# Kernel tuning notes

Measured on AMD Instinct MI355X. Metric: run time of the kernel, lower is better.

Reference implementation:

```python
import jax, jax.numpy as jnp
import numpy as np

N_HEAD = 16
N_EMBD = 1024

def setup_inputs() -> dict:
    key = jax.random.key(0)
    ks = jax.random.split(key, 7)
    B, S, D = 2, 2048, N_EMBD
    scale = 1.0 / np.sqrt(D)
    return {
        "x": jax.random.normal(ks[0], (B, S, D), dtype=jnp.float32),
        "Wq": jax.random.normal(ks[1], (D, D), dtype=jnp.float32) * scale,
        "bq": jnp.zeros((D,), dtype=jnp.float32),
        "Wk": jax.random.normal(ks[2], (D, D), dtype=jnp.float32) * scale,
        "bk": jnp.zeros((D,), dtype=jnp.float32),
        "Wv": jax.random.normal(ks[3], (D, D), dtype=jnp.float32) * scale,
        "bv": jnp.zeros((D,), dtype=jnp.float32),
    }

def reference(x, Wq, bq, Wk, bk, Wv, bv):
    B, S, D = x.shape
    H = N_HEAD
    hd = D // H
    # QKV projections
    q = (x @ Wq + bq).reshape(B, S, H, hd).transpose(0, 2, 1, 3)  # [B,H,S,hd]
    k = (x @ Wk + bk).reshape(B, S, H, hd).transpose(0, 2, 1, 3)
    v = (x @ Wv + bv).reshape(B, S, H, hd).transpose(0, 2, 1, 3)
    # Note: original module defines a causal mask but never applies it.
    att = jnp.einsum("bhqd,bhkd->bhqk", q, k) * (1.0 / jnp.sqrt(hd).astype(x.dtype))
    att = jax.nn.softmax(att, axis=-1)
    y = jnp.einsum("bhqk,bhkd->bhqd", att, v)  # [B,H,S,hd]
    return y.transpose(0, 2, 1, 3).reshape(B, S, D)
```

## Files before the change

### kernel.cpp

```cpp
#include <hip/hip_runtime.h>


#define D_MODEL 1024
#define NHEAD   16
#define HDIM    64
#define SEQ     2048
#define MROWS   4096
#define CSC     0.18033688011112042f

typedef __attribute__((ext_vector_type(8))) short short8;
typedef __attribute__((ext_vector_type(4))) float f32x4;

__device__ __forceinline__ float bf2f(unsigned short u) {
  return __uint_as_float(((unsigned int)u) << 16);
}
__device__ __forceinline__ unsigned short f2bf(float f) {
  unsigned int u = __float_as_uint(f);
  u += 0x7fff + ((u >> 16) & 1);
  return (unsigned short)(u >> 16);
}
__device__ __forceinline__ unsigned int cvtpk_bf16(float lo, float hi) {
  unsigned int r;
  asm("v_cvt_pk_bf16_f32 %0, %1, %2" : "=v"(r) : "v"(lo), "v"(hi));
  return r;
}

__device__ __forceinline__ int sniff_bf16(const unsigned short* x) {
  int cnt = 0;
#pragma unroll
  for (int i = 0; i < 64; ++i) {
    const unsigned e = (x[2 * i] >> 7) & 0xFF;
    cnt += (e >= 105 && e <= 140) ? 1 : 0;
  }
  return cnt >= 48;
}

__device__ __forceinline__ void gl_lds16(const unsigned short* g, unsigned short* l) {
  __builtin_amdgcn_global_load_lds(
      (const __attribute__((address_space(1))) unsigned int*)g,
      (__attribute__((address_space(3))) unsigned int*)l, 16, 0, 0);
}

__global__ __launch_bounds__(256) void cvt_x(const unsigned short* __restrict__ X,
                                             unsigned short* __restrict__ Xbf) {
  const int isbf = sniff_bf16(X);
  const size_t i0 = ((size_t)blockIdx.x * 256 + threadIdx.x) * 8;
  if (isbf) {
    *(uint4*)(Xbf + i0) = *(const uint4*)(X + i0);
  } else {
    const float* Xf = (const float*)X;
    const float4 f0 = *(const float4*)(Xf + i0);
    const float4 f1 = *(const float4*)(Xf + i0 + 4);
    unsigned int t[4] = {cvtpk_bf16(f0.x, f0.y), cvtpk_bf16(f0.z, f0.w),
                         cvtpk_bf16(f1.x, f1.y), cvtpk_bf16(f1.z, f1.w)};
    *(uint4*)(Xbf + i0) = *(const uint4*)t;
  }
}

__global__ __launch_bounds__(256) void cvt_w(
    const unsigned short* __restrict__ w0, const unsigned short* __restrict__ w1,
    const unsigned short* __restrict__ w2,
    const unsigned short* __restrict__ b0, const unsigned short* __restrict__ b1,
    const unsigned short* __restrict__ b2,
    unsigned short* __restrict__ Wt, unsigned short* __restrict__ bb) {
  __shared__ unsigned short tile[32][33];
  const int z = blockIdx.z;
  const unsigned short* W    = (z == 0) ? w0 : ((z == 1) ? w1 : w2);
  const unsigned short* bias = (z == 0) ? b0 : ((z == 1) ? b1 : b2);
  unsigned short* Wtz = Wt + ((size_t)z << 20);
  const int isbf = sniff_bf16(W);
  const int bx = blockIdx.x * 32;
  const int by = blockIdx.y * 32;
  const int tx = threadIdx.x & 31;
  const int ty = threadIdx.x >> 5;
#pragma unroll
  for (int r = ty; r < 32; r += 8) {
    unsigned short v;
    if (isbf) v = W[(size_t)(by + r) * D_MODEL + bx + tx];
    else      v = f2bf(((const float*)W)[(size_t)(by + r) * D_MODEL + bx + tx]);
    tile[r][tx] = v;
  }
  __syncthreads();
#pragma unroll
  for (int r = ty; r < 32; r += 8)
    Wtz[(size_t)(bx + r) * D_MODEL + by + tx] = tile[tx][r];
  if (blockIdx.x == 0 && blockIdx.y == 0) {
    const int i0 = threadIdx.x * 4;
#pragma unroll
    for (int j = 0; j < 4; ++j)
      bb[z * D_MODEL + i0 + j] =
          isbf ? bias[i0 + j] : f2bf(((const float*)bias)[i0 + j]);
  }
}

__device__ __forceinline__ void store_cd(int z, unsigned short* Out, int row0,
                                         int col, const f32x4 acc, float bb,
                                         float sc) {
  if (z == 2) {
    const int b = row0 >> 11, s = row0 & 2047;
    const int bh = b * NHEAD + (col >> 6);
    uint2 pk;
    pk.x = cvtpk_bf16(acc[0] + bb, acc[1] + bb);
    pk.y = cvtpk_bf16(acc[2] + bb, acc[3] + bb);
    *(uint2*)(Out + ((size_t)bh * HDIM + (col & 63)) * SEQ + s) = pk;
  } else {
#pragma unroll
    for (int r = 0; r < 4; ++r)
      Out[(size_t)(row0 + r) * D_MODEL + col] = f2bf((acc[r] + bb) * sc);
  }
}

__global__ __launch_bounds__(256) void qkv_gemm_fast(
    const unsigned short* __restrict__ Xbf, const unsigned short* __restrict__ Wt,
    const unsigned short* __restrict__ bb,
    unsigned short* __restrict__ Oq, unsigned short* __restrict__ Ok,
    unsigned short* __restrict__ Ov) {
  const int z = blockIdx.z;
  const unsigned short* Wz = Wt + ((size_t)z << 20);
  unsigned short* Out = (z == 0) ? Oq : ((z == 1) ? Ok : Ov);
  const float sc = (z == 0) ? CSC : 1.0f;

  __shared__ unsigned short As[128 * 32];
  __shared__ unsigned short Bs[128 * 32];

  const int tid  = threadIdx.x;
  const int wave = tid >> 6, lane = tid & 63;
  const int wm = wave >> 1, wn = wave & 1;
  const int lrow = lane & 15, lk = lane >> 4;
  const int m0 = blockIdx.y * 128;
  const int n0 = blockIdx.x * 128;

  f32x4 acc[4][4] = {};

  for (int kk = 0; kk < D_MODEL; kk += 32) {
#pragma unroll
    for (int i = 0; i < 2; ++i) {
      const int c = i * 256 + tid;
      const int row = c >> 2, off = (c & 3) * 8;
      gl_lds16(Xbf + (size_t)(m0 + row) * D_MODEL + kk + off, &As[c * 8]);
      gl_lds16(Wz  + (size_t)(n0 + row) * D_MODEL + kk + off, &Bs[c * 8]);
    }
    __syncthreads();
    short8 a[4], b[4];
#pragma unroll
    for (int t = 0; t < 4; ++t) {
      a[t] = *(const short8*)(&As[(wm * 64 + t * 16 + lrow) * 32 + lk * 8]);
      b[t] = *(const short8*)(&Bs[(wn * 64 + t * 16 + lrow) * 32 + lk * 8]);
    }
#pragma unroll
    for (int mt = 0; mt < 4; ++mt)
#pragma unroll
      for (int nt = 0; nt < 4; ++nt)
        acc[mt][nt] = __builtin_amdgcn_mfma_f32_16x16x32_bf16(a[mt], b[nt], acc[mt][nt], 0, 0, 0);
    __syncthreads();
  }
#pragma unroll
  for (int nt = 0; nt < 4; ++nt) {
    const int col = n0 + wn * 64 + nt * 16 + lrow;
    const float bv = bf2f(bb[z * D_MODEL + col]);
#pragma unroll
    for (int mt = 0; mt < 4; ++mt)
      store_cd(z, Out, m0 + wm * 64 + mt * 16 + lk * 4, col, acc[mt][nt], bv, sc);
  }
}

#define LDA 40
__global__ __launch_bounds__(256) void qkv_gemm_med(
    const unsigned short* __restrict__ X, const unsigned short* __restrict__ Wt,
    const unsigned short* __restrict__ bb,
    unsigned short* __restrict__ Oq, unsigned short* __restrict__ Ok,
    unsigned short* __restrict__ Ov) {
  const int z = blockIdx.z;
  const unsigned short* Wz = Wt + ((size_t)z << 20);
  unsigned short* Out = (z == 0) ? Oq : ((z == 1) ? Ok : Ov);
  const float sc = (z == 0) ? CSC : 1.0f;

  __shared__ alignas(16) unsigned short As[128 * LDA];
  __shared__ alignas(16) unsigned short Bs[128 * LDA];

  const int isbf = sniff_bf16(X);
  const int tid  = threadIdx.x;
  const int wave = tid >> 6, lane = tid & 63;
  const int wm = wave >> 1, wn = wave & 1;
  const int lrow = lane & 15, lk = lane >> 4;
  const int m0 = blockIdx.y * 128;
  const int n0 = blockIdx.x * 128;

  f32x4 acc[4][4] = {};

  for (int kk = 0; kk < D_MODEL; kk += 32) {
#pragma unroll
    for (int i = 0; i < 2; ++i) {
      const int c = tid + i * 256;
      const int row = c >> 2, off = (c & 3) * 8;
      if (isbf) {
        *(uint4*)(&As[row * LDA + off]) =
            *(const uint4*)(X + (size_t)(m0 + row) * D_MODEL + kk + off);
      } else {
        const float* Xf = (const float*)X;
        const float4 f0 = *(const float4*)(Xf + (size_t)(m0 + row) * D_MODEL + kk + off);
        const float4 f1 = *(const float4*)(Xf + (size_t)(m0 + row) * D_MODEL + kk + off + 4);
        unsigned int t[4] = {cvtpk_bf16(f0.x, f0.y), cvtpk_bf16(f0.z, f0.w),
                             cvtpk_bf16(f1.x, f1.y), cvtpk_bf16(f1.z, f1.w)};
        *(uint4*)(&As[row * LDA + off]) = *(const uint4*)t;
      }
      *(uint4*)(&Bs[row * LDA + off]) =
          *(const uint4*)(Wz + (size_t)(n0 + row) * D_MODEL + kk + off);
    }
    __syncthreads();
    short8 a[4], b[4];
#pragma unroll
    for (int t = 0; t < 4; ++t) {
      a[t] = *(const short8*)(&As[(wm * 64 + t * 16 + lrow) * LDA + lk * 8]);
      b[t] = *(const short8*)(&Bs[(wn * 64 + t * 16 + lrow) * LDA + lk * 8]);
    }
#pragma unroll
    for (int mt = 0; mt < 4; ++mt)
#pragma unroll
      for (int nt = 0; nt < 4; ++nt)
        acc[mt][nt] = __builtin_amdgcn_mfma_f32_16x16x32_bf16(a[mt], b[nt], acc[mt][nt], 0, 0, 0);
    __syncthreads();
  }
#pragma unroll
  for (int nt = 0; nt < 4; ++nt) {
    const int col = n0 + wn * 64 + nt * 16 + lrow;
    const float bv = bf2f(bb[z * D_MODEL + col]);
#pragma unroll
    for (int mt = 0; mt < 4; ++mt)
      store_cd(z, Out, m0 + wm * 64 + mt * 16 + lk * 4, col, acc[mt][nt], bv, sc);
  }
}

__global__ __launch_bounds__(256) void qkv_gemm(
    const unsigned short* __restrict__ X,
    const unsigned short* __restrict__ Wq, const unsigned short* __restrict__ Wk,
    const unsigned short* __restrict__ Wv,
    const unsigned short* __restrict__ bq, const unsigned short* __restrict__ bk,
    const unsigned short* __restrict__ bv,
    unsigned short* __restrict__ Oq, unsigned short* __restrict__ Ok,
    unsigned short* __restrict__ Ov) {
  const int z = blockIdx.z;
  const unsigned short* W    = (z == 0) ? Wq : ((z == 1) ? Wk : Wv);
  const unsigned short* bias = (z == 0) ? bq : ((z == 1) ? bk : bv);
  unsigned short*       Out  = (z == 0) ? Oq : ((z == 1) ? Ok : Ov);
  const float sc = (z == 0) ? CSC : 1.0f;

  __shared__ alignas(16) unsigned short As[128 * LDA];
  __shared__ alignas(16) unsigned short Bs[128 * LDA];

  const int isbf = sniff_bf16(X);
  const int tid  = threadIdx.x;
  const int wave = tid >> 6, lane = tid & 63;
  const int wm = wave >> 1, wn = wave & 1;
  const int lrow = lane & 15, lk = lane >> 4;
  const int m0 = blockIdx.y * 128;
  const int n0 = blockIdx.x * 128;

  f32x4 acc[4][4] = {};

  for (int kk = 0; kk < D_MODEL; kk += 32) {
#pragma unroll
    for (int i = 0; i < 2; ++i) {
      const int c = tid + i * 256;
      const int row = c >> 2, off = (c & 3) * 8;
      if (isbf) {
        *(uint4*)(&As[row * LDA + off]) =
            *(const uint4*)(X + (size_t)(m0 + row) * D_MODEL + kk + off);
      } else {
        const float* Xf = (const float*)X;
        const float4 f0 = *(const float4*)(Xf + (size_t)(m0 + row) * D_MODEL + kk + off);
        const float4 f1 = *(const float4*)(Xf + (size_t)(m0 + row) * D_MODEL + kk + off + 4);
        unsigned int t[4] = {cvtpk_bf16(f0.x, f0.y), cvtpk_bf16(f0.z, f0.w),
                             cvtpk_bf16(f1.x, f1.y), cvtpk_bf16(f1.z, f1.w)};
        *(uint4*)(&As[row * LDA + off]) = *(const uint4*)t;
      }
    }
#pragma unroll
    for (int i = 0; i < 2; ++i) {
      const int c = tid + i * 256;
      const int krow = c & 31;
      const int nc0 = (c >> 5) * 8;
      if (isbf) {
        uint4 v = *(const uint4*)(W + (size_t)(kk + krow) * D_MODEL + n0 + nc0);
        const unsigned short* e = (const unsigned short*)&v;
#pragma unroll
        for (int j = 0; j < 8; ++j) Bs[(nc0 + j) * LDA + krow] = e[j];
      } else {
        const float* Wf = (const float*)W;
        const float4 f0 = *(const float4*)(Wf + (size_t)(kk + krow) * D_MODEL + n0 + nc0);
        const float4 f1 = *(const float4*)(Wf + (size_t)(kk + krow) * D_MODEL + n0 + nc0 + 4);
        const float vals[8] = {f0.x, f0.y, f0.z, f0.w, f1.x, f1.y, f1.z, f1.w};
#pragma unroll
        for (int j = 0; j < 8; ++j) Bs[(nc0 + j) * LDA + krow] = f2bf(vals[j]);
      }
    }
    __syncthreads();
    short8 a[4], b[4];
#pragma unroll
    for (int t = 0; t < 4; ++t) {
      a[t] = *(const short8*)(&As[(wm * 64 + t * 16 + lrow) * LDA + lk * 8]);
      b[t] = *(const short8*)(&Bs[(wn * 64 + t * 16 + lrow) * LDA + lk * 8]);
    }
#pragma unroll
    for (int mt = 0; mt < 4; ++mt)
#pragma unroll
      for (int nt = 0; nt < 4; ++nt)
        acc[mt][nt] = __builtin_amdgcn_mfma_f32_16x16x32_bf16(a[mt], b[nt], acc[mt][nt], 0, 0, 0);
    __syncthreads();
  }
#pragma unroll
  for (int nt = 0; nt < 4; ++nt) {
    const int col = n0 + wn * 64 + nt * 16 + lrow;
    const float bv2 = isbf ? bf2f(bias[col]) : ((const float*)bias)[col];
#pragma unroll
    for (int mt = 0; mt < 4; ++mt)
      store_cd(z, Out, m0 + wm * 64 + mt * 16 + lk * 4, col, acc[mt][nt], bv2, sc);
  }
}

#define LDK 72
__global__ __launch_bounds__(256) void attn(
    const unsigned short* __restrict__ Qg, const unsigned short* __restrict__ Kg,
    const unsigned short* __restrict__ Vtg, unsigned short* __restrict__ Outg,
    const unsigned short* __restrict__ Xs) {
  const int qt = blockIdx.x;
  const int bh = blockIdx.y;
  const int b = bh >> 4, h = bh & 15;
  const size_t baseR = (size_t)b * SEQ * D_MODEL + h * HDIM;
  const size_t baseV = (size_t)bh * HDIM * SEQ;

  __shared__ alignas(16) unsigned short Ks[64 * LDK];
  __shared__ alignas(16) unsigned short Vs[64 * LDK];
  __shared__ alignas(16) unsigned short Ps[128 * LDK];

  const int isbf = sniff_bf16(Xs);
  const int tid  = threadIdx.x;
  const int wave = tid >> 6, lane = tid & 63;
  const int lrow = lane & 15, lk = lane >> 4;
  const int q0 = qt * 128;
  const int wq = wave * 32;

  short8 qf[2][2];
#pragma unroll
  for (int nq = 0; nq < 2; ++nq)
#pragma unroll
    for (int ks = 0; ks < 2; ++ks)
      qf[nq][ks] = *(const short8*)(Qg + baseR +
          (size_t)(q0 + wq + nq * 16 + lrow) * D_MODEL + ks * 32 + lk * 8);

  f32x4 accO[2][4] = {};
  float lsum[2] = {0.f, 0.f};

  uint4 kreg[2], vreg[2];
  auto LOADT = [&](int kv) {
#pragma unroll
    for (int i = 0; i < 2; ++i) {
      const int c = tid + i * 256;
      const int row = c >> 3, off = (c & 7) * 8;
      kreg[i] = *(const uint4*)(Kg + baseR + (size_t)(kv + row) * D_MODEL + off);
      vreg[i] = *(const uint4*)(Vtg + baseV + (size_t)row * SEQ + kv + off);
    }
  };
  auto WRITET = [&]() {
#pragma unroll
    for (int i = 0; i < 2; ++i) {
      const int c = tid + i * 256;
      const int row = c >> 3, off = (c & 7) * 8;
      *(uint4*)(&Ks[row * LDK + off]) = kreg[i];
      *(uint4*)(&Vs[row * LDK + off]) = vreg[i];
    }
  };

  LOADT(0);
  WRITET();
  __syncthreads();

#pragma unroll 1
  for (int kv0 = 0; kv0 < SEQ; kv0 += 64) {
    const int nxt = kv0 + 64;
    if (nxt < SEQ) LOADT(nxt);

    f32x4 accST[4][2] = {};
#pragma unroll
    for (int ks = 0; ks < 2; ++ks) {
      short8 kf[4];
#pragma unroll
      for (int mt = 0; mt < 4; ++mt)
        kf[mt] = *(const short8*)(&Ks[(mt * 16 + lrow) * LDK + ks * 32 + lk * 8]);
#pragma unroll
      for (int mt = 0; mt < 4; ++mt)
#pragma unroll
        for (int nq = 0; nq < 2; ++nq)
          accST[mt][nq] = __builtin_amdgcn_mfma_f32_16x16x32_bf16(
              kf[mt], qf[nq][ks], accST[mt][nq], 0, 0, 0);
    }

#pragma unroll
    for (int mt = 0; mt < 4; ++mt)
#pragma unroll
      for (int nq = 0; nq < 2; ++nq) {
        const float p0 = exp2f(accST[mt][nq][0]), p1 = exp2f(accST[mt][nq][1]);
        const float p2 = exp2f(accST[mt][nq][2]), p3 = exp2f(accST[mt][nq][3]);
        lsum[nq] += (p0 + p1) + (p2 + p3);
        uint2 pk;
        pk.x = cvtpk_bf16(p0, p1);
        pk.y = cvtpk_bf16(p2, p3);
        *(uint2*)(&Ps[(wq + nq * 16 + lrow) * LDK + mt * 16 + lk * 4]) = pk;
      }

#pragma unroll
    for (int ks = 0; ks < 2; ++ks) {
      short8 pf[2], vf[4];
#pragma unroll
      for (int mq = 0; mq < 2; ++mq)
        pf[mq] = *(const short8*)(&Ps[(wq + mq * 16 + lrow) * LDK + ks * 32 + lk * 8]);
#pragma unroll
      for (int nd = 0; nd < 4; ++nd)
        vf[nd] = *(const short8*)(&Vs[(nd * 16 + lrow) * LDK + ks * 32 + lk * 8]);
#pragma unroll
      for (int mq = 0; mq < 2; ++mq)
#pragma unroll
        for (int nd = 0; nd < 4; ++nd)
          accO[mq][nd] = __builtin_amdgcn_mfma_f32_16x16x32_bf16(
              pf[mq], vf[nd], accO[mq][nd], 0, 0, 0);
    }

    __syncthreads();
    if (nxt < SEQ) WRITET();
    __syncthreads();
  }

#pragma unroll
  for (int nq = 0; nq < 2; ++nq) {
    lsum[nq] += __shfl_xor(lsum[nq], 16, 64);
    lsum[nq] += __shfl_xor(lsum[nq], 32, 64);
  }
  __syncthreads();
  float* Lf = (float*)Ps;
  if (lk == 0) {
    Lf[wq + lrow]      = lsum[0];
    Lf[wq + 16 + lrow] = lsum[1];
  }
#pragma unroll
  for (int mq = 0; mq < 2; ++mq) {
    const f32x4 l4 = *(const f32x4*)(&Lf[wq + mq * 16 + lk * 4]);
#pragma unroll
    for (int r = 0; r < 4; ++r) {
      const float inv = 1.0f / l4[r];
      const int row = q0 + wq + mq * 16 + lk * 4 + r;
#pragma unroll
      for (int nd = 0; nd < 4; ++nd) {
        const int col = h * HDIM + nd * 16 + lrow;
        const float val = accO[mq][nd][r] * inv;
        const size_t idx = (size_t)b * SEQ * D_MODEL + (size_t)row * D_MODEL + col;
        if (isbf) Outg[idx] = f2bf(val);
        else      ((float*)Outg)[idx] = val;
      }
    }
  }
}

extern "C" void kernel_launch(void* const* d_in, const int* in_sizes, int n_in,
                              void* d_out, int out_size, void* d_ws, size_t ws_size,
                              hipStream_t stream) {
  const unsigned short* x  = (const unsigned short*)d_in[0];
  const unsigned short* Wq = (const unsigned short*)d_in[1];
  const unsigned short* bq = (const unsigned short*)d_in[2];
  const unsigned short* Wk = (const unsigned short*)d_in[3];
  const unsigned short* bk = (const unsigned short*)d_in[4];
  const unsigned short* Wv = (const unsigned short*)d_in[5];
  const unsigned short* bv = (const unsigned short*)d_in[6];
  unsigned short* out = (unsigned short*)d_out;
  unsigned short* ws  = (unsigned short*)d_ws;

  const size_t M1 = 1u << 20;
  const size_t wsE = ws_size / 2;

  unsigned short* Wt  = ws;
  unsigned short* bb  = ws + 3 * M1;
  unsigned short* K   = ws + 3 * M1 + 65536;
  unsigned short* Vt  = K + 4 * M1;
  unsigned short* Xbf = Vt + 4 * M1;
  unsigned short* Q;

  if (wsE >= 19 * M1 + 65536) {
    Q = Xbf + 4 * M1;
    cvt_x<<<dim3(2048), 256, 0, stream>>>(x, Xbf);
    cvt_w<<<dim3(32, 32, 3), 256, 0, stream>>>(Wq, Wk, Wv, bq, bk, bv, Wt, bb);
    qkv_gemm_fast<<<dim3(8, 32, 3), 256, 0, stream>>>(Xbf, Wt, bb, Q, K, Vt);
  } else if (wsE >= 15 * M1 + 65536) {
    Q = out;
    cvt_x<<<dim3(2048), 256, 0, stream>>>(x, Xbf);
    cvt_w<<<dim3(32, 32, 3), 256, 0, stream>>>(Wq, Wk, Wv, bq, bk, bv, Wt, bb);
    qkv_gemm_fast<<<dim3(8, 32, 3), 256, 0, stream>>>(Xbf, Wt, bb, Q, K, Vt);
  } else if (wsE >= 11 * M1 + 65536) {
    Q = out;
    cvt_w<<<dim3(32, 32, 3), 256, 0, stream>>>(Wq, Wk, Wv, bq, bk, bv, Wt, bb);
    qkv_gemm_med<<<dim3(8, 32, 3), 256, 0, stream>>>(x, Wt, bb, Q, K, Vt);
  } else {
    if (wsE >= 12 * M1) { Q = ws; K = ws + 4 * M1; Vt = ws + 8 * M1; }
    else                { Q = out; K = ws; Vt = ws + 4 * M1; }
    qkv_gemm<<<dim3(8, 32, 3), 256, 0, stream>>>(x, Wq, Wk, Wv, bq, bk, bv, Q, K, Vt);
  }
  attn<<<dim3(16, 32), 256, 0, stream>>>(Q, K, Vt, out, x);
}
```

Measured before the change: 227.4 us.

## Double-buffer K/V tiles in attention to drop one barrier per step

Splits the shared K and V tiles into A/B ping-pong buffers so the next tile is written into the idle buffer right after compute, instead of waiting behind a barrier. This cuts each KV step to a single __syncthreads. The loop is unrolled by two with precomputed global pointers. It uses more LDS, which may lower occupancy.

```diff
diff --git a/kernel.cpp b/kernel.cpp
--- a/kernel.cpp
+++ b/kernel.cpp
@@ -319,6 +319,66 @@
 }
 
 #define LDK 72
+
+#define ATTN_STEP(KSC, VSC, KSN, VSN, PRE, NXT)                                \
+  {                                                                            \
+    if (PRE) {         \
+      ka = *(const uint4*)(Kg0 + (size_t)(NXT) * D_MODEL);                     \
+      kb = *(const uint4*)(Kg1 + (size_t)(NXT) * D_MODEL);                     \
+      va = *(const uint4*)(Vg0 + (NXT));                                       \
+      vb = *(const uint4*)(Vg1 + (NXT));                                       \
+    }                                                                          \
+    f32x4 accST[4][2] = {};                                                    \
+    _Pragma("unroll")                                                          \
+    for (int ks = 0; ks < 2; ++ks) {                                           \
+      short8 kf[4];                                                            \
+      _Pragma("unroll")                                                        \
+      for (int mt = 0; mt < 4; ++mt)                                           \
+        kf[mt] = *(const short8*)(&(KSC)[(mt * 16 + lrow) * LDK + ks * 32 + lk * 8]); \
+      _Pragma("unroll")                                                        \
+      for (int mt = 0; mt < 4; ++mt)                                           \
+        _Pragma("unroll")                                                      \
+        for (int nq = 0; nq < 2; ++nq)                                         \
+          accST[mt][nq] = __builtin_amdgcn_mfma_f32_16x16x32_bf16(             \
+              kf[mt], qf[nq][ks], accST[mt][nq], 0, 0, 0);                     \
+    }                                                                          \
+    _Pragma("unroll")                                                          \
+    for (int mt = 0; mt < 4; ++mt)                                             \
+      _Pragma("unroll")                                                        \
+      for (int nq = 0; nq < 2; ++nq) {                                         \
+        const float p0 = exp2f(accST[mt][nq][0]), p1 = exp2f(accST[mt][nq][1]);\
+        const float p2 = exp2f(accST[mt][nq][2]), p3 = exp2f(accST[mt][nq][3]);\
+        lsum[nq] += (p0 + p1) + (p2 + p3);                                     \
+        uint2 pk;                                                              \
+        pk.x = cvtpk_bf16(p0, p1);                                             \
+        pk.y = cvtpk_bf16(p2, p3);                                             \
+        *(uint2*)(&Ps[(wq + nq * 16 + lrow) * LDK + mt * 16 + lk * 4]) = pk;   \
+      }                                                                        \
+    _Pragma("unroll")                                                          \
+    for (int ks = 0; ks < 2; ++ks) {                                           \
+      short8 pf[2], vf[4];                                                     \
+      _Pragma("unroll")                                                        \
+      for (int mq = 0; mq < 2; ++mq)                                           \
+        pf[mq] = *(const short8*)(&Ps[(wq + mq * 16 + lrow) * LDK + ks * 32 + lk * 8]); \
+      _Pragma("unroll")                                                        \
+      for (int nd = 0; nd < 4; ++nd)                                           \
+        vf[nd] = *(const short8*)(&(VSC)[(nd * 16 + lrow) * LDK + ks * 32 + lk * 8]); \
+      _Pragma("unroll")                                                        \
+      for (int mq = 0; mq < 2; ++mq)                                           \
+        _Pragma("unroll")                                                      \
+        for (int nd = 0; nd < 4; ++nd)                                         \
+          accO[mq][nd] = __builtin_amdgcn_mfma_f32_16x16x32_bf16(              \
+              pf[mq], vf[nd], accO[mq][nd], 0, 0, 0);                          \
+    }                                                                          \
+    if (PRE) {        \
+      *(uint4*)(&(KSN)[r0 * LDK + o0]) = ka;                                   \
+      *(uint4*)(&(KSN)[r1 * LDK + o1]) = kb;                                   \
+      *(uint4*)(&(VSN)[r0 * LDK + o0]) = va;                                   \
+      *(uint4*)(&(VSN)[r1 * LDK + o1]) = vb;                                   \
+    }                                                                          \
+    __syncthreads();                                                           \
+  }
+
 __global__ __launch_bounds__(256) void attn(
     const unsigned short* __restrict__ Qg, const unsigned short* __restrict__ Kg,
     const unsigned short* __restrict__ Vtg, unsigned short* __restrict__ Outg,
@@ -329,8 +389,10 @@
   const size_t baseR = (size_t)b * SEQ * D_MODEL + h * HDIM;
   const size_t baseV = (size_t)bh * HDIM * SEQ;
 
-  __shared__ alignas(16) unsigned short Ks[64 * LDK];
-  __shared__ alignas(16) unsigned short Vs[64 * LDK];
+  __shared__ alignas(16) unsigned short KsA[64 * LDK];
+  __shared__ alignas(16) unsigned short KsB[64 * LDK];
+  __shared__ alignas(16) unsigned short VsA[64 * LDK];
+  __shared__ alignas(16) unsigned short VsB[64 * LDK];
   __shared__ alignas(16) unsigned short Ps[128 * LDK];
 
   const int isbf = sniff_bf16(Xs);
@@ -340,6 +402,13 @@
   const int q0 = qt * 128;
   const int wq = wave * 32;
 
+  const int c0 = tid,       r0 = c0 >> 3, o0 = (c0 & 7) * 8;
+  const int c1 = tid + 256, r1 = c1 >> 3, o1 = (c1 & 7) * 8;
+  const unsigned short* Kg0 = Kg  + baseR + (size_t)r0 * D_MODEL + o0;
+  const unsigned short* Kg1 = Kg  + baseR + (size_t)r1 * D_MODEL + o1;
+  const unsigned short* Vg0 = Vtg + baseV + (size_t)r0 * SEQ + o0;
+  const unsigned short* Vg1 = Vtg + baseV + (size_t)r1 * SEQ + o1;
+
   short8 qf[2][2];
 #pragma unroll
   for (int nq = 0; nq < 2; ++nq)
@@ -351,83 +420,22 @@
   f32x4 accO[2][4] = {};
   float lsum[2] = {0.f, 0.f};
 
-  uint4 kreg[2], vreg[2];
-  auto LOADT = [&](int kv) {
-#pragma unroll
-    for (int i = 0; i < 2; ++i) {
-      const int c = tid + i * 256;
-      const int row = c >> 3, off = (c & 7) * 8;
-      kreg[i] = *(const uint4*)(Kg + baseR + (size_t)(kv + row) * D_MODEL + off);
-      vreg[i] = *(const uint4*)(Vtg + baseV + (size_t)row * SEQ + kv + off);
-    }
-  };
-  auto WRITET = [&]() {
-#pragma unroll
-    for (int i = 0; i < 2; ++i) {
-      const int c = tid + i * 256;
-      const int row = c >> 3, off = (c & 7) * 8;
-      *(uint4*)(&Ks[row * LDK + off]) = kreg[i];
-      *(uint4*)(&Vs[row * LDK + off]) = vreg[i];
-    }
-  };
-
-  LOADT(0);
-  WRITET();
+  uint4 ka, kb, va, vb;
+
+  ka = *(const uint4*)(Kg0);
+  kb = *(const uint4*)(Kg1);
+  va = *(const uint4*)(Vg0);
+  vb = *(const uint4*)(Vg1);
+  *(uint4*)(&KsA[r0 * LDK + o0]) = ka;
+  *(uint4*)(&KsA[r1 * LDK + o1]) = kb;
+  *(uint4*)(&VsA[r0 * LDK + o0]) = va;
+  *(uint4*)(&VsA[r1 * LDK + o1]) = vb;
   __syncthreads();
 
 #pragma unroll 1
-  for (int kv0 = 0; kv0 < SEQ; kv0 += 64) {
-    const int nxt = kv0 + 64;
-    if (nxt < SEQ) LOADT(nxt);
-
-    f32x4 accST[4][2] = {};
-#pragma unroll
-    for (int ks = 0; ks < 2; ++ks) {
-      short8 kf[4];
-#pragma unroll
-      for (int mt = 0; mt < 4; ++mt)
-        kf[mt] = *(const short8*)(&Ks[(mt * 16 + lrow) * LDK + ks * 32 + lk * 8]);
-#pragma unroll
-      for (int mt = 0; mt < 4; ++mt)
-#pragma unroll
-        for (int nq = 0; nq < 2; ++nq)
-          accST[mt][nq] = __builtin_amdgcn_mfma_f32_16x16x32_bf16(
-              kf[mt], qf[nq][ks], accST[mt][nq], 0, 0, 0);
-    }
-
-#pragma unroll
-    for (int mt = 0; mt < 4; ++mt)
-#pragma unroll
-      for (int nq = 0; nq < 2; ++nq) {
-        const float p0 = exp2f(accST[mt][nq][0]), p1 = exp2f(accST[mt][nq][1]);
-        const float p2 = exp2f(accST[mt][nq][2]), p3 = exp2f(accST[mt][nq][3]);
-        lsum[nq] += (p0 + p1) + (p2 + p3);
-        uint2 pk;
-        pk.x = cvtpk_bf16(p0, p1);
-        pk.y = cvtpk_bf16(p2, p3);
-        *(uint2*)(&Ps[(wq + nq * 16 + lrow) * LDK + mt * 16 + lk * 4]) = pk;
-      }
-
-#pragma unroll
-    for (int ks = 0; ks < 2; ++ks) {
-      short8 pf[2], vf[4];
-#pragma unroll
-      for (int mq = 0; mq < 2; ++mq)
-        pf[mq] = *(const short8*)(&Ps[(wq + mq * 16 + lrow) * LDK + ks * 32 + lk * 8]);
-#pragma unroll
-      for (int nd = 0; nd < 4; ++nd)
-        vf[nd] = *(const short8*)(&Vs[(nd * 16 + lrow) * LDK + ks * 32 + lk * 8]);
-#pragma unroll
-      for (int mq = 0; mq < 2; ++mq)
-#pragma unroll
-        for (int nd = 0; nd < 4; ++nd)
-          accO[mq][nd] = __builtin_amdgcn_mfma_f32_16x16x32_bf16(
-              pf[mq], vf[nd], accO[mq][nd], 0, 0, 0);
-    }
-
-    __syncthreads();
-    if (nxt < SEQ) WRITET();
-    __syncthreads();
+  for (int kv0 = 0; kv0 < SEQ; kv0 += 128) {
+    ATTN_STEP(KsA, VsA, KsB, VsB, 1, kv0 + 64);
+    ATTN_STEP(KsB, VsB, KsA, VsA, (kv0 + 128 < SEQ), kv0 + 128);
   }
 
 #pragma unroll
```

Result: faster. 219.0 us (-3.7%).

## Halve attention query tile, double grid, add XCD-aware block remap

Applied to the files above, without the earlier changes.

The attention kernel now handles 64 query rows per block (16 per wave) instead of 128, so the grid doubles to 1024 blocks. Block indices are remapped so that all query tiles of the same batch-head land on the same XCD, which should improve L2 reuse of K/V. The register-prefetch double buffering of K/V is dropped in favour of direct global-to-LDS copies between two barriers, and launch bounds request 4 blocks per CU. In exchange, each K/V tile is loaded twice as often in total, MFMA reuse per K/V fragment is lower, and the load latency is no longer hidden by prefetch.

```diff
diff --git a/kernel.cpp b/kernel.cpp
--- a/kernel.cpp
+++ b/kernel.cpp
@@ -319,68 +319,53 @@
 }
 
 #define LDK 72
-__global__ __launch_bounds__(256) void attn(
+__global__ __launch_bounds__(256, 4) void attn(
     const unsigned short* __restrict__ Qg, const unsigned short* __restrict__ Kg,
     const unsigned short* __restrict__ Vtg, unsigned short* __restrict__ Outg,
     const unsigned short* __restrict__ Xs) {
-  const int qt = blockIdx.x;
-  const int bh = blockIdx.y;
+  const int lin = blockIdx.y * 32 + blockIdx.x;
+  const int xcd = lin & 7, idx = lin >> 3;
+  const int bh = xcd * 4 + (idx >> 5);
+  const int qt = idx & 31;
   const int b = bh >> 4, h = bh & 15;
   const size_t baseR = (size_t)b * SEQ * D_MODEL + h * HDIM;
   const size_t baseV = (size_t)bh * HDIM * SEQ;
 
   __shared__ alignas(16) unsigned short Ks[64 * LDK];
   __shared__ alignas(16) unsigned short Vs[64 * LDK];
-  __shared__ alignas(16) unsigned short Ps[128 * LDK];
+  __shared__ alignas(16) unsigned short Ps[64 * LDK];
 
   const int isbf = sniff_bf16(Xs);
   const int tid  = threadIdx.x;
   const int wave = tid >> 6, lane = tid & 63;
   const int lrow = lane & 15, lk = lane >> 4;
-  const int q0 = qt * 128;
-  const int wq = wave * 32;
-
-  short8 qf[2][2];
-#pragma unroll
-  for (int nq = 0; nq < 2; ++nq)
-#pragma unroll
-    for (int ks = 0; ks < 2; ++ks)
-      qf[nq][ks] = *(const short8*)(Qg + baseR +
-          (size_t)(q0 + wq + nq * 16 + lrow) * D_MODEL + ks * 32 + lk * 8);
-
-  f32x4 accO[2][4] = {};
-  float lsum[2] = {0.f, 0.f};
-
-  uint4 kreg[2], vreg[2];
-  auto LOADT = [&](int kv) {
+  const int q0 = qt * 64;
+  const int wq = wave * 16;
+
+  short8 qf[2];
+#pragma unroll
+  for (int ks = 0; ks < 2; ++ks)
+    qf[ks] = *(const short8*)(Qg + baseR +
+        (size_t)(q0 + wq + lrow) * D_MODEL + ks * 32 + lk * 8);
+
+  f32x4 accO[4] = {};
+  float lsum = 0.f;
+
+#pragma unroll 1
+  for (int kv0 = 0; kv0 < SEQ; kv0 += 64) {
+    __syncthreads();
 #pragma unroll
     for (int i = 0; i < 2; ++i) {
       const int c = tid + i * 256;
       const int row = c >> 3, off = (c & 7) * 8;
-      kreg[i] = *(const uint4*)(Kg + baseR + (size_t)(kv + row) * D_MODEL + off);
-      vreg[i] = *(const uint4*)(Vtg + baseV + (size_t)row * SEQ + kv + off);
-    }
-  };
-  auto WRITET = [&]() {
-#pragma unroll
-    for (int i = 0; i < 2; ++i) {
-      const int c = tid + i * 256;
-      const int row = c >> 3, off = (c & 7) * 8;
-      *(uint4*)(&Ks[row * LDK + off]) = kreg[i];
-      *(uint4*)(&Vs[row * LDK + off]) = vreg[i];
-    }
-  };
-
-  LOADT(0);
-  WRITET();
-  __syncthreads();
-
-#pragma unroll 1
-  for (int kv0 = 0; kv0 < SEQ; kv0 += 64) {
-    const int nxt = kv0 + 64;
-    if (nxt < SEQ) LOADT(nxt);
-
-    f32x4 accST[4][2] = {};
+      *(uint4*)(&Ks[row * LDK + off]) =
+          *(const uint4*)(Kg + baseR + (size_t)(kv0 + row) * D_MODEL + off);
+      *(uint4*)(&Vs[row * LDK + off]) =
+          *(const uint4*)(Vtg + baseV + (size_t)row * SEQ + kv0 + off);
+    }
+    __syncthreads();
+
+    f32x4 accST[4] = {};
 #pragma unroll
     for (int ks = 0; ks < 2; ++ks) {
       short8 kf[4];
@@ -389,73 +374,53 @@
         kf[mt] = *(const short8*)(&Ks[(mt * 16 + lrow) * LDK + ks * 32 + lk * 8]);
 #pragma unroll
       for (int mt = 0; mt < 4; ++mt)
-#pragma unroll
-        for (int nq = 0; nq < 2; ++nq)
-          accST[mt][nq] = __builtin_amdgcn_mfma_f32_16x16x32_bf16(
-              kf[mt], qf[nq][ks], accST[mt][nq], 0, 0, 0);
-    }
-
-#pragma unroll
-    for (int mt = 0; mt < 4; ++mt)
-#pragma unroll
-      for (int nq = 0; nq < 2; ++nq) {
-        const float p0 = exp2f(accST[mt][nq][0]), p1 = exp2f(accST[mt][nq][1]);
-        const float p2 = exp2f(accST[mt][nq][2]), p3 = exp2f(accST[mt][nq][3]);
-        lsum[nq] += (p0 + p1) + (p2 + p3);
-        uint2 pk;
-        pk.x = cvtpk_bf16(p0, p1);
-        pk.y = cvtpk_bf16(p2, p3);
-        *(uint2*)(&Ps[(wq + nq * 16 + lrow) * LDK + mt * 16 + lk * 4]) = pk;
-      }
+        accST[mt] = __builtin_amdgcn_mfma_f32_16x16x32_bf16(
+            kf[mt], qf[ks], accST[mt], 0, 0, 0);
+    }
+
+#pragma unroll
+    for (int mt = 0; mt < 4; ++mt) {
+      const float p0 = exp2f(accST[mt][0]), p1 = exp2f(accST[mt][1]);
+      const float p2 = exp2f(accST[mt][2]), p3 = exp2f(accST[mt][3]);
+      lsum += (p0 + p1) + (p2 + p3);
+      uint2 pk;
+      pk.x = cvtpk_bf16(p0, p1);
+      pk.y = cvtpk_bf16(p2, p3);
+      *(uint2*)(&Ps[(wq + lrow) * LDK + mt * 16 + lk * 4]) = pk;
+    }
 
 #pragma unroll
     for (int ks = 0; ks < 2; ++ks) {
-      short8 pf[2], vf[4];
-#pragma unroll
-      for (int mq = 0; mq < 2; ++mq)
-        pf[mq] = *(const short8*)(&Ps[(wq + mq * 16 + lrow) * LDK + ks * 32 + lk * 8]);
+      short8 vf[4];
+      const short8 pf = *(const short8*)(&Ps[(wq + lrow) * LDK + ks * 32 + lk * 8]);
 #pragma unroll
       for (int nd = 0; nd < 4; ++nd)
         vf[nd] = *(const short8*)(&Vs[(nd * 16 + lrow) * LDK + ks * 32 + lk * 8]);
 #pragma unroll
-      for (int mq = 0; mq < 2; ++mq)
-#pragma unroll
-        for (int nd = 0; nd < 4; ++nd)
-          accO[mq][nd] = __builtin_amdgcn_mfma_f32_16x16x32_bf16(
-              pf[mq], vf[nd], accO[mq][nd], 0, 0, 0);
-    }
-
-    __syncthreads();
-    if (nxt < SEQ) WRITET();
-    __syncthreads();
-  }
-
-#pragma unroll
-  for (int nq = 0; nq < 2; ++nq) {
-    lsum[nq] += __shfl_xor(lsum[nq], 16, 64);
-    lsum[nq] += __shfl_xor(lsum[nq], 32, 64);
-  }
+      for (int nd = 0; nd < 4; ++nd)
+        accO[nd] = __builtin_amdgcn_mfma_f32_16x16x32_bf16(
+            pf, vf[nd], accO[nd], 0, 0, 0);
+    }
+  }
+
+  lsum += __shfl_xor(lsum, 16, 64);
+  lsum += __shfl_xor(lsum, 32, 64);
   __syncthreads();
   float* Lf = (float*)Ps;
-  if (lk == 0) {
-    Lf[wq + lrow]      = lsum[0];
-    Lf[wq + 16 + lrow] = lsum[1];
-  }
-#pragma unroll
-  for (int mq = 0; mq < 2; ++mq) {
-    const f32x4 l4 = *(const f32x4*)(&Lf[wq + mq * 16 + lk * 4]);
-#pragma unroll
-    for (int r = 0; r < 4; ++r) {
-      const float inv = 1.0f / l4[r];
-      const int row = q0 + wq + mq * 16 + lk * 4 + r;
-#pragma unroll
-      for (int nd = 0; nd < 4; ++nd) {
-        const int col = h * HDIM + nd * 16 + lrow;
-        const float val = accO[mq][nd][r] * inv;
-        const size_t idx = (size_t)b * SEQ * D_MODEL + (size_t)row * D_MODEL + col;
-        if (isbf) Outg[idx] = f2bf(val);
-        else      ((float*)Outg)[idx] = val;
-      }
+  if (lk == 0) Lf[wq + lrow] = lsum;
+  __syncthreads();
+  const f32x4 l4 = *(const f32x4*)(&Lf[wq + lk * 4]);
+#pragma unroll
+  for (int r = 0; r < 4; ++r) {
+    const float inv = 1.0f / l4[r];
+    const int row = q0 + wq + lk * 4 + r;
+#pragma unroll
+    for (int nd = 0; nd < 4; ++nd) {
+      const int col = h * HDIM + nd * 16 + lrow;
+      const float val = accO[nd][r] * inv;
+      const size_t idx = (size_t)b * SEQ * D_MODEL + (size_t)row * D_MODEL + col;
+      if (isbf) Outg[idx] = f2bf(val);
+      else      ((float*)Outg)[idx] = val;
     }
   }
 }
@@ -502,5 +467,5 @@
     else                { Q = out; K = ws; Vt = ws + 4 * M1; }
     qkv_gemm<<<dim3(8, 32, 3), 256, 0, stream>>>(x, Wq, Wk, Wv, bq, bk, bv, Q, K, Vt);
   }
-  attn<<<dim3(16, 32), 256, 0, stream>>>(Q, K, Vt, out, x);
-}
+  attn<<<dim3(32, 32), 256, 0, stream>>>(Q, K, Vt, out, x);
+}
```

New measurement: 206.9 us. 9.0% less time.
